# Optimization experiments

Hardware: AMD Instinct MI355X
Metric: run time of the kernel (lower is better)

The kernel has to match this reference:

```python
import jax, jax.numpy as jnp
import numpy as np

H = 1024
N_HEAD = 16
HEAD = H // N_HEAD
EPS = 1e-12


def setup_inputs() -> dict:
    key = jax.random.key(0)
    ks = jax.random.split(key, 12)
    B, S = 2, 2048
    scale = 1.0 / np.sqrt(H)
    inp = {
        "pre_out": jax.random.normal(ks[0], (B, S, H), dtype=jnp.float32),
        "att_mask": jnp.ones((B, 1, 1, S), dtype=jnp.float32),
        "Wq": jax.random.normal(ks[1], (H, H), dtype=jnp.float32) * scale,
        "bq": jnp.zeros((H,), dtype=jnp.float32),
        "Wk": jax.random.normal(ks[2], (H, H), dtype=jnp.float32) * scale,
        "bk": jnp.zeros((H,), dtype=jnp.float32),
        "Wv": jax.random.normal(ks[3], (H, H), dtype=jnp.float32) * scale,
        "bv": jnp.zeros((H,), dtype=jnp.float32),
        "Wo": jax.random.normal(ks[4], (H, H), dtype=jnp.float32) * scale,
        "bo": jnp.zeros((H,), dtype=jnp.float32),
        "ln_w": jnp.ones((H,), dtype=jnp.float32),
        "ln_b": jnp.zeros((H,), dtype=jnp.float32),
    }
    return inp


def _heads(x):
    # [B,S,H] -> [B,n_head,S,head]
    B, S, _ = x.shape
    return x.reshape(B, S, N_HEAD, HEAD).transpose(0, 2, 1, 3)


def _layernorm(x, w, b):
    u = jnp.mean(x, axis=-1, keepdims=True)
    s = jnp.mean((x - u) ** 2, axis=-1, keepdims=True)
    return w * ((x - u) / jnp.sqrt(s + EPS)) + b


def reference(pre_out, att_mask, Wq, bq, Wk, bk, Wv, bv, Wo, bo, ln_w, ln_b):
    B, S, _ = pre_out.shape
    # torch Linear: y = x @ W.T + b
    Q = _heads(pre_out @ Wq.T + bq)
    K = _heads(pre_out @ Wk.T + bk)
    V = _heads(pre_out @ Wv.T + bv)
    scores = jnp.einsum('bhqd,bhkd->bhqk', Q, K) / np.sqrt(HEAD)
    scores = scores + (1.0 - att_mask) * -10000.0
    prob = jax.nn.softmax(scores, axis=-1)  # eval mode: no dropout
    att = jnp.einsum('bhqk,bhkd->bhqd', prob, V)
    att = att.transpose(0, 2, 1, 3).reshape(B, S, H)
    out = att @ Wo.T + bo
    return _layernorm(pre_out + out, ln_w, ln_b)
```

## Files before the change

### kernel.cpp

```cpp
#include <hip/hip_runtime.h>
#include <math.h>

typedef unsigned short u16;
typedef float floatx4 __attribute__((ext_vector_type(4)));
typedef __bf16 bf16x8 __attribute__((ext_vector_type(8)));
typedef u16 u16x4 __attribute__((ext_vector_type(4)));

#define BB 2
#define SS 2048
#define HH 1024
#define NHEAD 16

__device__ __forceinline__ u16 f2bf(float f) {
  union { float f; unsigned u; } a; a.f = f;
  unsigned r = a.u + 0x7fffu + ((a.u >> 16) & 1u);
  return (u16)(r >> 16);
}

__device__ __forceinline__ u16 bfbits(float f) {
  union { __bf16 h; u16 u; } c; c.h = (__bf16)f; return c.u;
}

__device__ __forceinline__ void gload16(const u16* g, u16* l) {
  __builtin_amdgcn_global_load_lds((const __attribute__((address_space(1))) void*)g,
                                   (__attribute__((address_space(3))) void*)l, 16, 0, 0);
}

__device__ __forceinline__ void fencebar() {
  asm volatile("" ::: "memory");
  __builtin_amdgcn_s_barrier();
  asm volatile("" ::: "memory");
}

__global__ __launch_bounds__(256) void cvt_all(
    const float* __restrict__ X, const float* __restrict__ Wq, const float* __restrict__ Wk,
    const float* __restrict__ Wv, const float* __restrict__ Wo, const float* __restrict__ mask,
    u16* __restrict__ Xb, u16* __restrict__ Wqb, u16* __restrict__ Wkb,
    u16* __restrict__ Wvb, u16* __restrict__ Wob, float* __restrict__ B2) {
  int i = blockIdx.x * 256 + threadIdx.x;
  if (i >= (2 << 20)) {
    int off = i - (2 << 20);
    float4 m = ((const float4*)mask)[off];
    float4 o;
    o.x = (1.0f - m.x) * (-10000.0f * 1.44269504f);
    o.y = (1.0f - m.y) * (-10000.0f * 1.44269504f);
    o.z = (1.0f - m.z) * (-10000.0f * 1.44269504f);
    o.w = (1.0f - m.w) * (-10000.0f * 1.44269504f);
    ((float4*)B2)[off] = o;
    return;
  }
  const float* src; u16* dst; int off;
  if (i < (1 << 20)) { src = X; dst = Xb; off = i; }
  else {
    int j = i - (1 << 20);
    int m = j >> 18; off = j & ((1 << 18) - 1);
    src = (m == 0) ? Wq : (m == 1) ? Wk : (m == 2) ? Wv : Wo;
    dst = (m == 0) ? Wqb : (m == 1) ? Wkb : (m == 2) ? Wvb : Wob;
  }
  float4 v = ((const float4*)src)[off];
  u16x4 p; p.x = f2bf(v.x); p.y = f2bf(v.y); p.z = f2bf(v.z); p.w = f2bf(v.w);
  ((u16x4*)dst)[off] = p;
}

__global__ __launch_bounds__(256) void qkv_gemm(
    const u16* __restrict__ X,
    const u16* __restrict__ Wq, const u16* __restrict__ Wk, const u16* __restrict__ Wv,
    const float* __restrict__ bq, const float* __restrict__ bk, const float* __restrict__ bv,
    u16* __restrict__ Qo, u16* __restrict__ Ko, u16* __restrict__ Vt) {
  __shared__ u16 As[128 * 32];
  __shared__ u16 Ws[128 * 32];

  const int tid = threadIdx.x;
  const int w = tid >> 6, lane = tid & 63, quad = lane >> 4, l15 = lane & 15;
  const int mat = blockIdx.x >> 3;
  const int col0 = (blockIdx.x & 7) * 128;
  const int row0 = blockIdx.y * 128;
  const u16* W = (mat == 0) ? Wq : (mat == 1) ? Wk : Wv;
  const float* bias = (mat == 0) ? bq : (mat == 1) ? bk : bv;

  const int c0 = tid, c1 = tid + 256;
  const int ar0 = c0 >> 2, al0 = ((c0 & 3) ^ (ar0 & 3)) * 8;
  const int ar1 = c1 >> 2, al1 = ((c1 & 3) ^ (ar1 & 3)) * 8;
  const u16* gA0 = X + (row0 + ar0) * HH + al0;
  const u16* gA1 = X + (row0 + ar1) * HH + al1;
  const u16* gW0 = W + (col0 + ar0) * HH + al0;
  const u16* gW1 = W + (col0 + ar1) * HH + al1;
  u16* lA0 = As + c0 * 8; u16* lA1 = As + c1 * 8;
  u16* lW0 = Ws + c0 * 8; u16* lW1 = Ws + c1 * 8;

  const int wm = (w >> 1) * 64, wn = (w & 1) * 64;
  const int sw = quad ^ (l15 & 3);
  const int aoff = (wm + l15) * 32 + sw * 8;
  const int boff = (wn + l15) * 32 + sw * 8;

  floatx4 acc[4][4];
#pragma unroll
  for (int i = 0; i < 4; i++)
#pragma unroll
    for (int j = 0; j < 4; j++) acc[i][j] = {0.f, 0.f, 0.f, 0.f};

  for (int k0 = 0; k0 < HH; k0 += 32) {
    __syncthreads();
    gload16(gA0 + k0, lA0);
    gload16(gA1 + k0, lA1);
    gload16(gW0 + k0, lW0);
    gload16(gW1 + k0, lW1);
    __syncthreads();
    bf16x8 af[4], bfr[4];
#pragma unroll
    for (int i = 0; i < 4; i++) af[i] = *(const bf16x8*)(As + aoff + i * 512);
#pragma unroll
    for (int j = 0; j < 4; j++) bfr[j] = *(const bf16x8*)(Ws + boff + j * 512);
#pragma unroll
    for (int i = 0; i < 4; i++)
#pragma unroll
      for (int j = 0; j < 4; j++)
        acc[i][j] = __builtin_amdgcn_mfma_f32_16x16x32_bf16(af[i], bfr[j], acc[i][j], 0, 0, 0);
  }

  const int rb = row0 + wm + quad * 4;
  if (mat < 2) {
    u16* O = (mat == 0) ? Qo : Ko;
#pragma unroll
    for (int j = 0; j < 4; j++) {
      const int col = col0 + wn + j * 16 + l15;
      const float bj = bias[col];
#pragma unroll
      for (int i = 0; i < 4; i++) {
        const int r0 = rb + i * 16;
#pragma unroll
        for (int r = 0; r < 4; r++)
          O[(r0 + r) * HH + col] = bfbits(acc[i][j][r] + bj);
      }
    }
  } else {
#pragma unroll
    for (int j = 0; j < 4; j++) {
      const int col = col0 + wn + j * 16 + l15;
      const float bj = bias[col];
      const int h = col >> 6, d = col & 63;
#pragma unroll
      for (int i = 0; i < 4; i++) {
        const int m0 = rb + i * 16;
        const int b = m0 >> 11, s = m0 & 2047;
        u16x4 pk;
#pragma unroll
        for (int r = 0; r < 4; r++) pk[r] = bfbits(acc[i][j][r] + bj);
        *(u16x4*)(Vt + (((b * NHEAD + h) * 64 + d) * SS + s)) = pk;
      }
    }
  }
}

__global__ __launch_bounds__(256) void oproj_gemm(
    const u16* __restrict__ A, const u16* __restrict__ W,
    const float* __restrict__ bias, float* __restrict__ Y) {
  __shared__ u16 As[128 * 32];
  __shared__ u16 Ws[64 * 32];

  const int tid = threadIdx.x;
  const int w = tid >> 6, lane = tid & 63, quad = lane >> 4, l15 = lane & 15;
  const int col0 = blockIdx.x * 64;
  const int row0 = blockIdx.y * 128;

  const int c0 = tid, c1 = tid + 256;
  const int ar0 = c0 >> 2, al0 = ((c0 & 3) ^ (ar0 & 3)) * 8;
  const int ar1 = c1 >> 2, al1 = ((c1 & 3) ^ (ar1 & 3)) * 8;
  const u16* gA0 = A + (row0 + ar0) * HH + al0;
  const u16* gA1 = A + (row0 + ar1) * HH + al1;
  const u16* gW0 = W + (col0 + ar0) * HH + al0;
  u16* lA0 = As + c0 * 8; u16* lA1 = As + c1 * 8;
  u16* lW0 = Ws + c0 * 8;

  const int wm = w * 32;
  const int sw = quad ^ (l15 & 3);
  const int aoff = (wm + l15) * 32 + sw * 8;
  const int boff = l15 * 32 + sw * 8;

  floatx4 acc[2][4];
#pragma unroll
  for (int i = 0; i < 2; i++)
#pragma unroll
    for (int j = 0; j < 4; j++) acc[i][j] = {0.f, 0.f, 0.f, 0.f};

  for (int k0 = 0; k0 < HH; k0 += 32) {
    __syncthreads();
    gload16(gA0 + k0, lA0);
    gload16(gA1 + k0, lA1);
    if (tid < 256) gload16(gW0 + k0, lW0);
    __syncthreads();
    bf16x8 af[2], bfr[4];
#pragma unroll
    for (int i = 0; i < 2; i++) af[i] = *(const bf16x8*)(As + aoff + i * 512);
#pragma unroll
    for (int j = 0; j < 4; j++) bfr[j] = *(const bf16x8*)(Ws + boff + j * 512);
#pragma unroll
    for (int i = 0; i < 2; i++)
#pragma unroll
      for (int j = 0; j < 4; j++)
        acc[i][j] = __builtin_amdgcn_mfma_f32_16x16x32_bf16(af[i], bfr[j], acc[i][j], 0, 0, 0);
  }

  const int rb = row0 + wm + quad * 4;
#pragma unroll
  for (int j = 0; j < 4; j++) {
    const int col = col0 + j * 16 + l15;
    const float bj = bias[col];
#pragma unroll
    for (int i = 0; i < 2; i++) {
      const int r0 = rb + i * 16;
#pragma unroll
      for (int r = 0; r < 4; r++)
        Y[(r0 + r) * HH + col] = acc[i][j][r] + bj;
    }
  }
}

#define QT 128

__global__ __launch_bounds__(256, 3) void attn_mfma(
    const u16* __restrict__ Q, const u16* __restrict__ K, const u16* __restrict__ Vt,
    const float* __restrict__ B2, u16* __restrict__ O) {
  __shared__ u16 UQ[9216];
  __shared__ u16 Ks[2][64 * 64];
  __shared__ u16 Vs[2][64 * 64];

  const int L = blockIdx.y * 16 + blockIdx.x;
  const int wid = (L & 7) * 64 + (L >> 3);
  const int qt = wid & 15, bh = wid >> 4;
  const int b = bh >> 4, h = bh & 15;
  const int tid = threadIdx.x;
  const int w = tid >> 6, lane = tid & 63, quad = lane >> 4, l15 = lane & 15;
  const int sw = l15 & 7;

  const int qbase  = (b * SS + qt * QT) * HH + h * 64;
  const int kvbase = (b * SS) * HH + h * 64;
  const int vtbase = (b * NHEAD + h) * 64 * SS;

  auto stage_kv = [&](u16* kd, u16* vd, int t) {
#pragma unroll
    for (int i = 0; i < 2; i++) {
      const int c = tid + i * 256;
      const int r = c >> 3, lc = (c & 7) ^ (r & 7);
      gload16(K + kvbase + (t * 64 + r) * HH + lc * 8, kd + c * 8);
      gload16(Vt + vtbase + r * SS + t * 64 + lc * 8, vd + c * 8);
    }
  };

#pragma unroll
  for (int i = 0; i < 4; i++) {
    const int c = tid + i * 256;
    const int r = c >> 3, lc = (c & 7) ^ (r & 7);
    gload16(Q + qbase + r * HH + lc * 8, UQ + c * 8);
  }
  stage_kv(Ks[0], Vs[0], 0);
  asm volatile("s_waitcnt vmcnt(4)" ::: "memory");
  fencebar();

  bf16x8 aQ[2][2];
#pragma unroll
  for (int mt = 0; mt < 2; mt++) {
    const u16* qr = UQ + (w * 32 + mt * 16 + l15) * 64;
    aQ[mt][0] = *(const bf16x8*)(qr + ((quad ^ sw) * 8));
    aQ[mt][1] = *(const bf16x8*)(qr + (((4 + quad) ^ sw) * 8));
  }

  floatx4 o[2][4];
#pragma unroll
  for (int mt = 0; mt < 2; mt++)
#pragma unroll
    for (int j = 0; j < 4; j++) o[mt][j] = {0.f, 0.f, 0.f, 0.f};
  float lp[2] = {0.f, 0.f};

  u16* Pw = UQ + w * 2304;
  const float* B2row = B2 + b * SS;

  for (int kt = 0; kt < 32; kt++) {
    const int cur = kt & 1;
    const u16* Kc = Ks[cur];
    const u16* Vc = Vs[cur];

    floatx4 bb[4];
#pragma unroll
    for (int kb = 0; kb < 4; kb++)
      bb[kb] = *(const floatx4*)(B2row + kt * 64 + kb * 16 + quad * 4);
    asm volatile("" ::: "memory");

    if (kt < 31) {
      stage_kv(Ks[cur ^ 1], Vs[cur ^ 1], kt + 1);
      asm volatile("s_waitcnt vmcnt(4) lgkmcnt(0)" ::: "memory");
    } else {
      asm volatile("s_waitcnt vmcnt(0) lgkmcnt(0)" ::: "memory");
    }
    fencebar();

    floatx4 st[2][4];
#pragma unroll
    for (int kb = 0; kb < 4; kb++) {
      const u16* kr = Kc + (kb * 16 + l15) * 64;
      bf16x8 kf0 = *(const bf16x8*)(kr + ((quad ^ sw) * 8));
      bf16x8 kf1 = *(const bf16x8*)(kr + (((4 + quad) ^ sw) * 8));
#pragma unroll
      for (int mt = 0; mt < 2; mt++) {
        floatx4 z = {0.f, 0.f, 0.f, 0.f};
        z = __builtin_amdgcn_mfma_f32_16x16x32_bf16(kf0, aQ[mt][0], z, 0, 0, 0);
        st[mt][kb] = __builtin_amdgcn_mfma_f32_16x16x32_bf16(kf1, aQ[mt][1], z, 0, 0, 0);
      }
    }

#pragma unroll
    for (int kb = 0; kb < 4; kb++) {
#pragma unroll
      for (int mt = 0; mt < 2; mt++) {
        u16x4 pk;
#pragma unroll
        for (int r = 0; r < 4; r++) {
          const float p = __builtin_amdgcn_exp2f(st[mt][kb][r] * 0.180336880f + bb[kb][r]);
          lp[mt] += p;
          pk[r] = bfbits(p);
        }
        *(u16x4*)(Pw + (mt * 16 + l15) * 72 + kb * 16 + quad * 4) = pk;
      }
    }

    bf16x8 pa[2][2];
#pragma unroll
    for (int mt = 0; mt < 2; mt++) {
      const u16* pr = Pw + (mt * 16 + l15) * 72;
      pa[mt][0] = *(const bf16x8*)(pr + quad * 8);
      pa[mt][1] = *(const bf16x8*)(pr + 32 + quad * 8);
    }
#pragma unroll
    for (int j = 0; j < 4; j++) {
      const u16* vr = Vc + (j * 16 + l15) * 64;
      bf16x8 v0 = *(const bf16x8*)(vr + ((quad ^ sw) * 8));
      bf16x8 v1 = *(const bf16x8*)(vr + (((4 + quad) ^ sw) * 8));
#pragma unroll
      for (int mt = 0; mt < 2; mt++) {
        o[mt][j] = __builtin_amdgcn_mfma_f32_16x16x32_bf16(pa[mt][0], v0, o[mt][j], 0, 0, 0);
        o[mt][j] = __builtin_amdgcn_mfma_f32_16x16x32_bf16(pa[mt][1], v1, o[mt][j], 0, 0, 0);
      }
    }

    fencebar();
  }

#pragma unroll
  for (int mt = 0; mt < 2; mt++) {
    float v = lp[mt];
    v += __shfl_xor(v, 16);
    v += __shfl_xor(v, 32);
    lp[mt] = v;
  }

#pragma unroll
  for (int mt = 0; mt < 2; mt++) {
    const int orow0 = b * SS + qt * QT + w * 32 + mt * 16 + quad * 4;
#pragma unroll
    for (int r = 0; r < 4; r++) {
      const float inv = 1.0f / __shfl(lp[mt], quad * 4 + r);
#pragma unroll
      for (int j = 0; j < 4; j++)
        O[(orow0 + r) * HH + h * 64 + j * 16 + l15] = bfbits(o[mt][j][r] * inv);
    }
  }
}

__device__ __forceinline__ float block_sum256(float v) {
  __shared__ float sb[4];
#pragma unroll
  for (int o = 1; o < 64; o <<= 1) v += __shfl_xor(v, o);
  if ((threadIdx.x & 63) == 0) sb[threadIdx.x >> 6] = v;
  __syncthreads();
  float r = sb[0] + sb[1] + sb[2] + sb[3];
  __syncthreads();
  return r;
}

__global__ __launch_bounds__(256) void add_layernorm(
    const float* __restrict__ x0, const float* __restrict__ y,
    const float* __restrict__ w, const float* __restrict__ b,
    float* __restrict__ out) {
  const int row = blockIdx.x;
  const int t = threadIdx.x;
  const float* xr = x0 + (size_t)row * HH;
  const float* yr = y + (size_t)row * HH;

  float v[4];
  float sum = 0.f;
#pragma unroll
  for (int i = 0; i < 4; i++) {
    int idx = t + i * 256;
    v[i] = xr[idx] + yr[idx];
    sum += v[i];
  }
  float mean = block_sum256(sum) * (1.0f / HH);

  float sq = 0.f;
#pragma unroll
  for (int i = 0; i < 4; i++) {
    float d = v[i] - mean;
    sq += d * d;
  }
  float var = block_sum256(sq) * (1.0f / HH);
  float inv = rsqrtf(var + 1e-12f);

#pragma unroll
  for (int i = 0; i < 4; i++) {
    int idx = t + i * 256;
    out[(size_t)row * HH + idx] = w[idx] * ((v[i] - mean) * inv) + b[idx];
  }
}

extern "C" void kernel_launch(void* const* d_in, const int* in_sizes, int n_in,
                              void* d_out, int out_size, void* d_ws, size_t ws_size,
                              hipStream_t stream) {
  const float* pre_out = (const float*)d_in[0];
  const float* mask    = (const float*)d_in[1];
  const float* Wq = (const float*)d_in[2];
  const float* bq = (const float*)d_in[3];
  const float* Wk = (const float*)d_in[4];
  const float* bk = (const float*)d_in[5];
  const float* Wv = (const float*)d_in[6];
  const float* bv = (const float*)d_in[7];
  const float* Wo = (const float*)d_in[8];
  const float* bo = (const float*)d_in[9];
  const float* ln_w = (const float*)d_in[10];
  const float* ln_b = (const float*)d_in[11];
  float* out = (float*)d_out;

  u16* Xb  = (u16*)d_ws;
  u16* Wqb = Xb + (4 << 20);
  u16* Wkb = Wqb + (1 << 20);
  u16* Wvb = Wkb + (1 << 20);
  u16* Wob = Wvb + (1 << 20);
  u16* Qb  = Wob + (1 << 20);
  u16* Kb  = Qb + (4 << 20);
  u16* Vtb = Kb + (4 << 20);
  u16* Ab  = Vtb + (4 << 20);
  float* Yb = (float*)(Ab + (4 << 20));
  float* B2 = Yb + (4 << 20);

  cvt_all<<<8196, 256, 0, stream>>>(pre_out, Wq, Wk, Wv, Wo, mask,
                                    Xb, Wqb, Wkb, Wvb, Wob, B2);

  qkv_gemm<<<dim3(24, 32), 256, 0, stream>>>(Xb, Wqb, Wkb, Wvb, bq, bk, bv, Qb, Kb, Vtb);

  attn_mfma<<<dim3(SS / QT, BB * NHEAD), 256, 0, stream>>>(Qb, Kb, Vtb, B2, Ab);

  oproj_gemm<<<dim3(16, 32), 256, 0, stream>>>(Ab, Wob, bo, Yb);

  add_layernorm<<<BB * SS, 256, 0, stream>>>(pre_out, Yb, ln_w, ln_b, out);
}
```

Measured before the change: 214.9 us.

## Split attention key tiles across two wave groups and swizzle GEMM block order

The attention kernel moves from 256 to 512 threads. Two groups of four waves each handle half of every 64-key tile for the same query rows, and their partial outputs and row sums are reduced through shared memory at the end. s_setprio hints are added around the MFMA sections. The QKV and output-projection GEMMs remap block indices with an XCD-style swizzle to improve L2 locality. The changes aim for more waves per CU and better cache reuse, at the cost of a shared-memory reduction step and more LDS per block.

```diff
diff --git a/kernel.cpp b/kernel.cpp
--- a/kernel.cpp
+++ b/kernel.cpp
@@ -72,9 +72,12 @@
 
   const int tid = threadIdx.x;
   const int w = tid >> 6, lane = tid & 63, quad = lane >> 4, l15 = lane & 15;
-  const int mat = blockIdx.x >> 3;
-  const int col0 = (blockIdx.x & 7) * 128;
-  const int row0 = blockIdx.y * 128;
+  const int L = blockIdx.y * 24 + blockIdx.x;
+  const int wid = (L & 7) * 96 + (L >> 3);
+  const int bx = wid % 24, by = wid / 24;
+  const int mat = bx >> 3;
+  const int col0 = (bx & 7) * 128;
+  const int row0 = by * 128;
   const u16* W = (mat == 0) ? Wq : (mat == 1) ? Wk : Wv;
   const float* bias = (mat == 0) ? bq : (mat == 1) ? bk : bv;
 
@@ -160,8 +163,10 @@
 
   const int tid = threadIdx.x;
   const int w = tid >> 6, lane = tid & 63, quad = lane >> 4, l15 = lane & 15;
-  const int col0 = blockIdx.x * 64;
-  const int row0 = blockIdx.y * 128;
+  const int L = blockIdx.y * 16 + blockIdx.x;
+  const int wid = (L & 7) * 64 + (L >> 3);
+  const int col0 = (wid & 15) * 64;
+  const int row0 = (wid >> 4) * 128;
 
   const int c0 = tid, c1 = tid + 256;
   const int ar0 = c0 >> 2, al0 = ((c0 & 3) ^ (ar0 & 3)) * 8;
@@ -218,12 +223,15 @@
 
 #define QT 128
 
-__global__ __launch_bounds__(256, 3) void attn_mfma(
+__global__ __launch_bounds__(512, 4) void attn_mfma(
     const u16* __restrict__ Q, const u16* __restrict__ K, const u16* __restrict__ Vt,
     const float* __restrict__ B2, u16* __restrict__ O) {
-  __shared__ u16 UQ[9216];
-  __shared__ u16 Ks[2][64 * 64];
-  __shared__ u16 Vs[2][64 * 64];
+  __shared__ u16 SMEM[26624];
+  u16* const UQ = SMEM;
+  u16* const KS0 = SMEM + 10240;
+  u16* const KS1 = SMEM + 14336;
+  u16* const VS0 = SMEM + 18432;
+  u16* const VS1 = SMEM + 22528;
 
   const int L = blockIdx.y * 16 + blockIdx.x;
   const int wid = (L & 7) * 64 + (L >> 3);
@@ -232,38 +240,40 @@
   const int tid = threadIdx.x;
   const int w = tid >> 6, lane = tid & 63, quad = lane >> 4, l15 = lane & 15;
   const int sw = l15 & 7;
+  const int qg = w & 3;
+  const int khalf = w >> 2;
+  const int koff = khalf * 32;
+  const int kh4 = khalf * 4;
 
   const int qbase  = (b * SS + qt * QT) * HH + h * 64;
   const int kvbase = (b * SS) * HH + h * 64;
   const int vtbase = (b * NHEAD + h) * 64 * SS;
 
   auto stage_kv = [&](u16* kd, u16* vd, int t) {
-#pragma unroll
-    for (int i = 0; i < 2; i++) {
-      const int c = tid + i * 256;
-      const int r = c >> 3, lc = (c & 7) ^ (r & 7);
-      gload16(K + kvbase + (t * 64 + r) * HH + lc * 8, kd + c * 8);
-      gload16(Vt + vtbase + r * SS + t * 64 + lc * 8, vd + c * 8);
-    }
+    const int c = tid;
+    const int r = c >> 3, lc = (c & 7) ^ (r & 7);
+    gload16(K + kvbase + (t * 64 + r) * HH + lc * 8, kd + c * 8);
+    gload16(Vt + vtbase + r * SS + t * 64 + lc * 8, vd + c * 8);
   };
 
 #pragma unroll
-  for (int i = 0; i < 4; i++) {
-    const int c = tid + i * 256;
+  for (int i = 0; i < 2; i++) {
+    const int c = tid + i * 512;
     const int r = c >> 3, lc = (c & 7) ^ (r & 7);
     gload16(Q + qbase + r * HH + lc * 8, UQ + c * 8);
   }
-  stage_kv(Ks[0], Vs[0], 0);
-  asm volatile("s_waitcnt vmcnt(4)" ::: "memory");
+  stage_kv(KS0, VS0, 0);
+  asm volatile("s_waitcnt vmcnt(2)" ::: "memory");
   fencebar();
 
   bf16x8 aQ[2][2];
 #pragma unroll
   for (int mt = 0; mt < 2; mt++) {
-    const u16* qr = UQ + (w * 32 + mt * 16 + l15) * 64;
+    const u16* qr = UQ + (qg * 32 + mt * 16 + l15) * 64;
     aQ[mt][0] = *(const bf16x8*)(qr + ((quad ^ sw) * 8));
     aQ[mt][1] = *(const bf16x8*)(qr + (((4 + quad) ^ sw) * 8));
   }
+  asm volatile("s_waitcnt lgkmcnt(0)" ::: "memory");
 
   floatx4 o[2][4];
 #pragma unroll
@@ -272,32 +282,33 @@
     for (int j = 0; j < 4; j++) o[mt][j] = {0.f, 0.f, 0.f, 0.f};
   float lp[2] = {0.f, 0.f};
 
-  u16* Pw = UQ + w * 2304;
+  u16* const Pw = UQ + w * 1280;
   const float* B2row = B2 + b * SS;
 
   for (int kt = 0; kt < 32; kt++) {
     const int cur = kt & 1;
-    const u16* Kc = Ks[cur];
-    const u16* Vc = Vs[cur];
-
-    floatx4 bb[4];
-#pragma unroll
-    for (int kb = 0; kb < 4; kb++)
-      bb[kb] = *(const floatx4*)(B2row + kt * 64 + kb * 16 + quad * 4);
+    const u16* Kc = cur ? KS1 : KS0;
+    const u16* Vc = cur ? VS1 : VS0;
+
+    const float* B2k = B2row + kt * 64 + koff;
+    floatx4 bb[2];
+    bb[0] = *(const floatx4*)(B2k + quad * 4);
+    bb[1] = *(const floatx4*)(B2k + 16 + quad * 4);
     asm volatile("" ::: "memory");
 
     if (kt < 31) {
-      stage_kv(Ks[cur ^ 1], Vs[cur ^ 1], kt + 1);
-      asm volatile("s_waitcnt vmcnt(4) lgkmcnt(0)" ::: "memory");
+      stage_kv(cur ? KS0 : KS1, cur ? VS0 : VS1, kt + 1);
+      asm volatile("s_waitcnt vmcnt(2)" ::: "memory");
     } else {
-      asm volatile("s_waitcnt vmcnt(0) lgkmcnt(0)" ::: "memory");
+      asm volatile("s_waitcnt vmcnt(0)" ::: "memory");
     }
     fencebar();
 
-    floatx4 st[2][4];
-#pragma unroll
-    for (int kb = 0; kb < 4; kb++) {
-      const u16* kr = Kc + (kb * 16 + l15) * 64;
+    floatx4 st[2][2];
+    __builtin_amdgcn_s_setprio(1);
+#pragma unroll
+    for (int kb = 0; kb < 2; kb++) {
+      const u16* kr = Kc + (koff + kb * 16 + l15) * 64;
       bf16x8 kf0 = *(const bf16x8*)(kr + ((quad ^ sw) * 8));
       bf16x8 kf1 = *(const bf16x8*)(kr + (((4 + quad) ^ sw) * 8));
 #pragma unroll
@@ -307,9 +318,10 @@
         st[mt][kb] = __builtin_amdgcn_mfma_f32_16x16x32_bf16(kf1, aQ[mt][1], z, 0, 0, 0);
       }
     }
-
-#pragma unroll
-    for (int kb = 0; kb < 4; kb++) {
+    __builtin_amdgcn_s_setprio(0);
+
+#pragma unroll
+    for (int kb = 0; kb < 2; kb++) {
 #pragma unroll
       for (int mt = 0; mt < 2; mt++) {
         u16x4 pk;
@@ -319,28 +331,24 @@
           lp[mt] += p;
           pk[r] = bfbits(p);
         }
-        *(u16x4*)(Pw + (mt * 16 + l15) * 72 + kb * 16 + quad * 4) = pk;
+        *(u16x4*)(Pw + (mt * 16 + l15) * 40 + kb * 16 + quad * 4) = pk;
       }
     }
 
-    bf16x8 pa[2][2];
-#pragma unroll
-    for (int mt = 0; mt < 2; mt++) {
-      const u16* pr = Pw + (mt * 16 + l15) * 72;
-      pa[mt][0] = *(const bf16x8*)(pr + quad * 8);
-      pa[mt][1] = *(const bf16x8*)(pr + 32 + quad * 8);
-    }
+    bf16x8 pa[2];
+#pragma unroll
+    for (int mt = 0; mt < 2; mt++)
+      pa[mt] = *(const bf16x8*)(Pw + (mt * 16 + l15) * 40 + quad * 8);
+    __builtin_amdgcn_s_setprio(1);
 #pragma unroll
     for (int j = 0; j < 4; j++) {
       const u16* vr = Vc + (j * 16 + l15) * 64;
-      bf16x8 v0 = *(const bf16x8*)(vr + ((quad ^ sw) * 8));
-      bf16x8 v1 = *(const bf16x8*)(vr + (((4 + quad) ^ sw) * 8));
-#pragma unroll
-      for (int mt = 0; mt < 2; mt++) {
-        o[mt][j] = __builtin_amdgcn_mfma_f32_16x16x32_bf16(pa[mt][0], v0, o[mt][j], 0, 0, 0);
-        o[mt][j] = __builtin_amdgcn_mfma_f32_16x16x32_bf16(pa[mt][1], v1, o[mt][j], 0, 0, 0);
-      }
-    }
+      bf16x8 vf = *(const bf16x8*)(vr + (((kh4 + quad) ^ sw) * 8));
+#pragma unroll
+      for (int mt = 0; mt < 2; mt++)
+        o[mt][j] = __builtin_amdgcn_mfma_f32_16x16x32_bf16(pa[mt], vf, o[mt][j], 0, 0, 0);
+    }
+    __builtin_amdgcn_s_setprio(0);
 
     fencebar();
   }
@@ -353,15 +361,41 @@
     lp[mt] = v;
   }
 
-#pragma unroll
-  for (int mt = 0; mt < 2; mt++) {
-    const int orow0 = b * SS + qt * QT + w * 32 + mt * 16 + quad * 4;
-#pragma unroll
-    for (int r = 0; r < 4; r++) {
-      const float inv = 1.0f / __shfl(lp[mt], quad * 4 + r);
+  float* const oS  = (float*)(SMEM + 10240);
+  float* const lpS = (float*)SMEM;
+  if (w >= 4) {
+    float* pb = oS + (w - 4) * 2048;
+#pragma unroll
+    for (int mt = 0; mt < 2; mt++) {
 #pragma unroll
       for (int j = 0; j < 4; j++)
-        O[(orow0 + r) * HH + h * 64 + j * 16 + l15] = bfbits(o[mt][j][r] * inv);
+#pragma unroll
+        for (int r = 0; r < 4; r++)
+          pb[(mt * 16 + quad * 4 + r) * 64 + j * 16 + l15] = o[mt][j][r];
+      if (quad == 0) lpS[qg * 32 + mt * 16 + l15] = lp[mt];
+    }
+  }
+  asm volatile("s_waitcnt lgkmcnt(0)" ::: "memory");
+  fencebar();
+
+  if (w < 4) {
+    const float* pb = oS + w * 2048;
+    float lpt[2];
+#pragma unroll
+    for (int mt = 0; mt < 2; mt++)
+      lpt[mt] = lp[mt] + lpS[w * 32 + mt * 16 + l15];
+#pragma unroll
+    for (int mt = 0; mt < 2; mt++) {
+      const int orow0 = b * SS + qt * QT + qg * 32 + mt * 16 + quad * 4;
+#pragma unroll
+      for (int r = 0; r < 4; r++) {
+        const float inv = 1.0f / __shfl(lpt[mt], quad * 4 + r);
+#pragma unroll
+        for (int j = 0; j < 4; j++) {
+          const float val = o[mt][j][r] + pb[(mt * 16 + quad * 4 + r) * 64 + j * 16 + l15];
+          O[(orow0 + r) * HH + h * 64 + j * 16 + l15] = bfbits(val * inv);
+        }
+      }
     }
   }
 }
@@ -446,7 +480,7 @@
 
   qkv_gemm<<<dim3(24, 32), 256, 0, stream>>>(Xb, Wqb, Wkb, Wvb, bq, bk, bv, Qb, Kb, Vtb);
 
-  attn_mfma<<<dim3(SS / QT, BB * NHEAD), 256, 0, stream>>>(Qb, Kb, Vtb, B2, Ab);
+  attn_mfma<<<dim3(SS / QT, BB * NHEAD), 512, 0, stream>>>(Qb, Kb, Vtb, B2, Ab);
 
   oproj_gemm<<<dim3(16, 32), 256, 0, stream>>>(Ab, Wob, bo, Yb);
 
```

New measurement: 202.8 us. 1.06x faster.
